# Optimization experiments

Hardware: AMD Instinct MI355X
Metric: run time of the kernel (lower is better)

Reference implementation:

```python
import jax, jax.numpy as jnp
import numpy as np

N_NODES = 50000
N_EDGES = 800000
IN_DIM = 128
HIDDEN = 128
OUT_DIM = 64


def setup_inputs() -> dict:
    key = jax.random.key(0)
    ks = jax.random.split(key, 10)
    x = jax.random.normal(ks[0], (N_NODES, IN_DIM), dtype=jnp.float32)
    edge_index = jax.random.randint(ks[1], (2, N_EDGES), 0, N_NODES, dtype=jnp.int64)
    def lin(k, fan_in, fan_out):
        bound = 1.0 / np.sqrt(fan_in)
        kw, kb = jax.random.split(k)
        W = jax.random.uniform(kw, (fan_in, fan_out), jnp.float32, -bound, bound)
        b = jax.random.uniform(kb, (fan_out,), jnp.float32, -bound, bound)
        return W, b
    W1, b1 = lin(ks[2], IN_DIM, HIDDEN)   # gcn layer 1
    W2, b2 = lin(ks[3], HIDDEN, HIDDEN)   # gcn layer 2
    W3, b3 = lin(ks[4], HIDDEN, HIDDEN)   # post_mp linear 1
    W4, b4 = lin(ks[5], HIDDEN, OUT_DIM)  # post_mp linear 2
    return {"x": x, "edge_index": edge_index,
            "W1": W1, "b1": b1, "W2": W2, "b2": b2,
            "W3": W3, "b3": b3, "W4": W4, "b4": b4}


def reference(x, edge_index, W1, b1, W2, b2, W3, b3, W4, b4):
    N = x.shape[0]
    # add self-loops (matches convert_to_adj)
    loops = jnp.arange(N, dtype=edge_index.dtype)
    row = jnp.concatenate([edge_index[0], loops])  # destination / adj row
    col = jnp.concatenate([edge_index[1], loops])  # source / adj col
    # row-normalization: vals = 1 / deg(row), deg from scatter-add of ones
    deg = jax.ops.segment_sum(jnp.ones(row.shape[0], x.dtype), row, num_segments=N)
    vals = 1.0 / deg[row]  # [E+N]

    def propagate(h):
        # SpMM: out[i] = sum_j A_norm[i,j] * h[j]  via gather-scale-scatter
        return jax.ops.segment_sum(vals[:, None] * h[col], row, num_segments=N)

    # layer 1: spmm -> linear -> relu (dropout is identity in eval mode)
    h = jax.nn.relu(propagate(x) @ W1 + b1)
    # layer 2
    h = jax.nn.relu(propagate(h) @ W2 + b2)
    # post_mp: Linear -> Dropout(eval=identity) -> Linear
    h = h @ W3 + b3
    return h @ W4 + b4
```

## Files before the change

kernel.cpp:

```cpp
#include <hip/hip_runtime.h>
#include <hip/hip_bf16.h>

#define NB 512

typedef __attribute__((ext_vector_type(8))) short short8_t;
typedef __attribute__((ext_vector_type(8))) unsigned short ushort8_t;
typedef __attribute__((ext_vector_type(4))) float f32x4;

__device__ inline unsigned short bf16_rne(float f) {
    union { float f; unsigned u; } x; x.f = f;
    unsigned r = x.u + 0x7fffu + ((x.u >> 16) & 1u);
    return (unsigned short)(r >> 16);
}
__device__ inline float bf16_to_f32(unsigned short h) {
    union { unsigned u; float f; } x; x.u = ((unsigned)h) << 16;
    return x.f;
}


__global__ __launch_bounds__(256) void p0_count_k(const int* __restrict__ e_row, int E, int R,
                                                  int* __restrict__ bucket_cnt) {
    __shared__ int h[NB];
    for (int i = threadIdx.x; i < NB; i += 256) h[i] = 0;
    __syncthreads();
    int base = blockIdx.x * 4096;
#pragma unroll
    for (int j = 0; j < 16; ++j) {
        int i = base + j * 256 + threadIdx.x;
        if (i < E) atomicAdd(&h[e_row[i] / R], 1);
    }
    __syncthreads();
    for (int i = threadIdx.x; i < NB; i += 256)
        if (h[i]) atomicAdd(&bucket_cnt[i], h[i]);
}


__global__ void p0b_scan_k(const int* __restrict__ cnt, int* __restrict__ bptr,
                           int* __restrict__ bcur, int E) {
    __shared__ int s[NB];
    int t = threadIdx.x;
    int v = cnt[t];
    s[t] = v;
    __syncthreads();
    for (int off = 1; off < NB; off <<= 1) {
        int u = (t >= off) ? s[t - off] : 0;
        __syncthreads();
        s[t] += u;
        __syncthreads();
    }
    int excl = s[t] - v;
    bptr[t] = excl;
    bcur[t] = excl;
    if (t == NB - 1) bptr[NB] = E;
}


__global__ __launch_bounds__(256) void p1_scatter_k(const int* __restrict__ er,
                                                    const int* __restrict__ ec, int E, int R,
                                                    int* __restrict__ bcur,
                                                    unsigned* __restrict__ packed) {
    __shared__ int h[NB];
    __shared__ int base[NB];
    for (int i = threadIdx.x; i < NB; i += 256) h[i] = 0;
    __syncthreads();
    int cb = blockIdx.x * 4096;
    int rows[16], cols[16], bks[16];
#pragma unroll
    for (int j = 0; j < 16; ++j) {
        int i = cb + j * 256 + threadIdx.x;
        if (i < E) {
            int r = er[i];
            rows[j] = r;
            cols[j] = ec[i];
            int b = r / R;
            bks[j] = b;
            atomicAdd(&h[b], 1);
        } else {
            bks[j] = -1;
        }
    }
    __syncthreads();
    for (int i = threadIdx.x; i < NB; i += 256)
        base[i] = h[i] ? atomicAdd(&bcur[i], h[i]) : 0;
    __syncthreads();
    for (int i = threadIdx.x; i < NB; i += 256) h[i] = 0;
    __syncthreads();
#pragma unroll
    for (int j = 0; j < 16; ++j) {
        int b = bks[j];
        if (b >= 0) {
            int off = atomicAdd(&h[b], 1);
            packed[base[b] + off] = ((unsigned)(rows[j] - b * R) << 16) | (unsigned)cols[j];
        }
    }
}


__global__ __launch_bounds__(256) void p2_build_k(const unsigned* __restrict__ packed,
                                                  const int* __restrict__ bptr, int R, int N, int E,
                                                  int* __restrict__ row_ptr,
                                                  float* __restrict__ deginv,
                                                  int* __restrict__ csr_col) {
    __shared__ int hist[128];
    __shared__ int excl[129];
    __shared__ int cur[128];
    __shared__ int lcsr[2048];
    int b = blockIdx.x;
    int s = bptr[b], e = bptr[b + 1];
    int m = e - s;
    for (int i = threadIdx.x; i < 128; i += 256) hist[i] = 0;
    __syncthreads();
    for (int i = threadIdx.x; i < m; i += 256) atomicAdd(&hist[packed[s + i] >> 16], 1);
    __syncthreads();
    if (threadIdx.x == 0) {
        int acc = 0;
        for (int r = 0; r < R; ++r) { excl[r] = acc; acc += hist[r]; }
        excl[R] = acc;
    }
    __syncthreads();
    for (int r = threadIdx.x; r < R; r += 256) {
        int gr = b * R + r;
        if (gr < N) {
            row_ptr[gr] = s + excl[r];
            deginv[gr] = 1.0f / (float)(hist[r] + 1);
        }
        cur[r] = excl[r];
    }
    if (b == (int)gridDim.x - 1 && threadIdx.x == 0) row_ptr[N] = E;
    __syncthreads();
    if (m <= 2048) {
        for (int i = threadIdx.x; i < m; i += 256) {
            unsigned pk = packed[s + i];
            int pos = atomicAdd(&cur[pk >> 16], 1);
            lcsr[pos] = (int)(pk & 0xffffu);
        }
        __syncthreads();
        for (int i = threadIdx.x; i < m; i += 256) csr_col[s + i] = lcsr[i];
    } else {
        for (int i = threadIdx.x; i < m; i += 256) {
            unsigned pk = packed[s + i];
            int pos = atomicAdd(&cur[pk >> 16], 1);
            csr_col[s + pos] = (int)(pk & 0xffffu);
        }
    }
}


__global__ void prep_weights_k(const float* __restrict__ W1, const float* __restrict__ W2,
                               const float* __restrict__ W3, const float* __restrict__ b3,
                               const float* __restrict__ W4, const float* __restrict__ b4,
                               unsigned short* __restrict__ w1t, unsigned short* __restrict__ w2t,
                               unsigned short* __restrict__ wft, float* __restrict__ bfv) {
    int idx = blockIdx.x * 256 + threadIdx.x;
    if (idx < 16384) {
        int k = idx >> 7, c = idx & 127;
        w1t[c * 128 + k] = bf16_rne(W1[idx]);
    } else if (idx < 32768) {
        int j = idx - 16384;
        int k = j >> 7, c = j & 127;
        w2t[c * 128 + k] = bf16_rne(W2[j]);
    } else if (idx < 40960) {
        int j = idx - 32768;
        int k = j >> 6, o = j & 63;
        float acc = 0.f;
        for (int m = 0; m < 128; ++m) acc = fmaf(W3[k * 128 + m], W4[m * 64 + o], acc);
        wft[o * 128 + k] = bf16_rne(acc);
    } else if (idx < 41024) {
        int o = idx - 40960;
        float acc = b4[o];
        for (int m = 0; m < 128; ++m) acc = fmaf(b3[m], W4[m * 64 + o], acc);
        bfv[o] = acc;
    }
}


template <int NC, bool OUT_BF16, bool IN_F32>
__global__ __launch_bounds__(256) void gemm_bf16_k(const void* __restrict__ Ain,
                                                   const unsigned short* __restrict__ Wt,
                                                   const float* __restrict__ bias,
                                                   void* __restrict__ Cout, int n) {
    constexpr int CT = NC / 16;
    __shared__ unsigned short As[64 * 128];
    const int t = threadIdx.x;
    const int row0 = blockIdx.x * 64;

    if (IN_F32) {
        const float* A = (const float*)Ain;
#pragma unroll
        for (int it = 0; it < 4; ++it) {
            int idx = it * 2048 + t * 8;
            int rl = idx >> 7;
            int cl = idx & 127;
            int gr = row0 + rl; if (gr > n - 1) gr = n - 1;
            const float4* src = (const float4*)(A + (size_t)gr * 128 + cl);
            float4 v0 = src[0];
            float4 v1 = src[1];
            float f[8] = {v0.x, v0.y, v0.z, v0.w, v1.x, v1.y, v1.z, v1.w};
            ushort8_t vh;
#pragma unroll
            for (int j = 0; j < 8; ++j) vh[j] = bf16_rne(f[j]);
            int byte = rl * 256 + ((cl * 2) ^ ((rl & 7) << 4));
            *(ushort8_t*)((char*)As + byte) = vh;
        }
    } else {
        const char* Ab = (const char*)((const unsigned short*)Ain + (size_t)row0 * 128);
#pragma unroll
        for (int it = 0; it < 4; ++it) {
            int dst = it * 4096 + t * 16;
            int rl = dst >> 8;
            int off = dst & 255;
            int src = rl * 256 + (off ^ ((rl & 7) << 4));
            __builtin_amdgcn_global_load_lds(
                (const __attribute__((address_space(1))) void*)(Ab + src),
                (__attribute__((address_space(3))) void*)((char*)As + dst), 16, 0, 0);
        }
    }
    __syncthreads();

    const int w = t >> 6;
    const int l = t & 63;
    const int col = l & 15;
    const int kg = l >> 4;
    const int arow = w * 16 + col;
    const int abase = arow * 256;
    const int axor = (arow & 7) << 4;

    short8_t afrag[4];
#pragma unroll
    for (int ks = 0; ks < 4; ++ks) {
        int abyte = abase + ((ks * 64 + kg * 16) ^ axor);
        afrag[ks] = *(const short8_t*)((const char*)As + abyte);
    }

    f32x4 acc[CT];
#pragma unroll
    for (int ct = 0; ct < CT; ++ct) acc[ct] = (f32x4){0.f, 0.f, 0.f, 0.f};

#pragma unroll
    for (int ct = 0; ct < CT; ++ct) {
        const unsigned short* wp = Wt + (size_t)(ct * 16 + col) * 128 + kg * 8;
#pragma unroll
        for (int ks = 0; ks < 4; ++ks) {
            short8_t b = *(const short8_t*)(wp + ks * 32);
            acc[ct] = __builtin_amdgcn_mfma_f32_16x16x32_bf16(afrag[ks], b, acc[ct], 0, 0, 0);
        }
    }

    const int orow0 = row0 + w * 16 + kg * 4;
    if (OUT_BF16) {
        unsigned short* C = (unsigned short*)Cout;
#pragma unroll
        for (int ct = 0; ct < CT; ++ct) {
#pragma unroll
            for (int j = 0; j < 4; ++j) {
                C[(size_t)(orow0 + j) * NC + ct * 16 + col] = bf16_rne(acc[ct][j]);
            }
        }
    } else {
        float* C = (float*)Cout;
#pragma unroll
        for (int ct = 0; ct < CT; ++ct) {
            float b = (bias != nullptr) ? bias[ct * 16 + col] : 0.f;
#pragma unroll
            for (int j = 0; j < 4; ++j) {
                int r = orow0 + j;
                if (r < n) C[(size_t)r * NC + ct * 16 + col] = acc[ct][j] + b;
            }
        }
    }
}


__global__ __launch_bounds__(256) void spmm_k(const unsigned short* __restrict__ t,
                                              const int* __restrict__ row_ptr,
                                              const int* __restrict__ csr_col,
                                              const float* __restrict__ deg_inv,
                                              const float* __restrict__ bias,
                                              unsigned short* __restrict__ out, int n) {
    int wave = threadIdx.x >> 6;
    int lane = threadIdx.x & 63;
    int half = lane >> 5;
    int sl = lane & 31;
    int row = blockIdx.x * 8 + wave * 2 + half;
    if (row >= n) return;

    const uint2* tw = (const uint2*)t;
    uint2 sv = tw[(size_t)row * 32 + sl];
    float a0 = bf16_to_f32((unsigned short)(sv.x & 0xffff));
    float a1 = bf16_to_f32((unsigned short)(sv.x >> 16));
    float a2 = bf16_to_f32((unsigned short)(sv.y & 0xffff));
    float a3 = bf16_to_f32((unsigned short)(sv.y >> 16));

    int s = row_ptr[row], e = row_ptr[row + 1];
    int p = s;
    for (; p + 4 <= e; p += 4) {
        int c0 = csr_col[p + 0];
        int c1 = csr_col[p + 1];
        int c2 = csr_col[p + 2];
        int c3 = csr_col[p + 3];
        uint2 v0 = tw[(size_t)c0 * 32 + sl];
        uint2 v1 = tw[(size_t)c1 * 32 + sl];
        uint2 v2 = tw[(size_t)c2 * 32 + sl];
        uint2 v3 = tw[(size_t)c3 * 32 + sl];
        a0 += bf16_to_f32((unsigned short)(v0.x & 0xffff)) + bf16_to_f32((unsigned short)(v1.x & 0xffff)) +
              bf16_to_f32((unsigned short)(v2.x & 0xffff)) + bf16_to_f32((unsigned short)(v3.x & 0xffff));
        a1 += bf16_to_f32((unsigned short)(v0.x >> 16)) + bf16_to_f32((unsigned short)(v1.x >> 16)) +
              bf16_to_f32((unsigned short)(v2.x >> 16)) + bf16_to_f32((unsigned short)(v3.x >> 16));
        a2 += bf16_to_f32((unsigned short)(v0.y & 0xffff)) + bf16_to_f32((unsigned short)(v1.y & 0xffff)) +
              bf16_to_f32((unsigned short)(v2.y & 0xffff)) + bf16_to_f32((unsigned short)(v3.y & 0xffff));
        a3 += bf16_to_f32((unsigned short)(v0.y >> 16)) + bf16_to_f32((unsigned short)(v1.y >> 16)) +
              bf16_to_f32((unsigned short)(v2.y >> 16)) + bf16_to_f32((unsigned short)(v3.y >> 16));
    }
    for (; p < e; ++p) {
        int c = csr_col[p];
        uint2 v = tw[(size_t)c * 32 + sl];
        a0 += bf16_to_f32((unsigned short)(v.x & 0xffff));
        a1 += bf16_to_f32((unsigned short)(v.x >> 16));
        a2 += bf16_to_f32((unsigned short)(v.y & 0xffff));
        a3 += bf16_to_f32((unsigned short)(v.y >> 16));
    }

    float di = deg_inv[row];
    float4 b = ((const float4*)bias)[sl];
    float r0 = fmaxf(fmaf(a0, di, b.x), 0.f);
    float r1 = fmaxf(fmaf(a1, di, b.y), 0.f);
    float r2 = fmaxf(fmaf(a2, di, b.z), 0.f);
    float r3 = fmaxf(fmaf(a3, di, b.w), 0.f);
    uint2 pk;
    pk.x = (unsigned)bf16_rne(r0) | ((unsigned)bf16_rne(r1) << 16);
    pk.y = (unsigned)bf16_rne(r2) | ((unsigned)bf16_rne(r3) << 16);
    ((uint2*)out)[(size_t)row * 32 + sl] = pk;
}


extern "C" void kernel_launch(void* const* d_in, const int* in_sizes, int n_in,
                              void* d_out, int out_size, void* d_ws, size_t ws_size,
                              hipStream_t stream) {
    const float* x  = (const float*)d_in[0];
    const int* edges = (const int*)d_in[1];
    const float* W1 = (const float*)d_in[2];
    const float* b1 = (const float*)d_in[3];
    const float* W2 = (const float*)d_in[4];
    const float* b2 = (const float*)d_in[5];
    const float* W3 = (const float*)d_in[6];
    const float* b3 = (const float*)d_in[7];
    const float* W4 = (const float*)d_in[8];
    const float* b4 = (const float*)d_in[9];

    const int N = in_sizes[0] / 128;
    const int E = in_sizes[1] / 2;
    const int NPAD = (N + 63) & ~63;
    const int R = (N + NB - 1) / NB;
    const int* e_row = edges;
    const int* e_col = edges + E;

    char* p = (char*)d_ws;
    auto alloc = [&](size_t bytes) {
        void* r = (void*)p;
        p += (bytes + 255) & ~(size_t)255;
        return r;
    };
    unsigned short* t_bf = (unsigned short*)alloc((size_t)NPAD * 128 * 2);
    unsigned short* h_bf = (unsigned short*)alloc((size_t)NPAD * 128 * 2);
    float* deginv  = (float*)alloc((size_t)N * 4);
    int*   row_ptr = (int*)alloc((size_t)(N + 1) * 4);
    int*   csr_col = (int*)alloc((size_t)E * 4);
    unsigned* packed = (unsigned*)alloc((size_t)E * 4);
    int*   bucket_cnt = (int*)alloc(NB * 4);
    int*   bucket_ptr = (int*)alloc((NB + 1) * 4);
    int*   bucket_cur = (int*)alloc(NB * 4);
    unsigned short* w1t = (unsigned short*)alloc(128 * 128 * 2);
    unsigned short* w2t = (unsigned short*)alloc(128 * 128 * 2);
    unsigned short* wft = (unsigned short*)alloc(64 * 128 * 2);
    float* bfv     = (float*)alloc(64 * 4);

    float* out = (float*)d_out;

    hipMemsetAsync(bucket_cnt, 0, NB * 4, stream);

    const int echunks = (E + 4095) / 4096;
    p0_count_k<<<echunks, 256, 0, stream>>>(e_row, E, R, bucket_cnt);
    p0b_scan_k<<<1, NB, 0, stream>>>(bucket_cnt, bucket_ptr, bucket_cur, E);
    p1_scatter_k<<<echunks, 256, 0, stream>>>(e_row, e_col, E, R, bucket_cur, packed);
    p2_build_k<<<NB, 256, 0, stream>>>(packed, bucket_ptr, R, N, E, row_ptr, deginv, csr_col);
    prep_weights_k<<<(41024 + 255) / 256, 256, 0, stream>>>(W1, W2, W3, b3, W4, b4,
                                                            w1t, w2t, wft, bfv);

    const int gblocks = NPAD / 64;

    gemm_bf16_k<128, true, true><<<gblocks, 256, 0, stream>>>(x, w1t, nullptr, t_bf, N);
    spmm_k<<<(N + 7) / 8, 256, 0, stream>>>(t_bf, row_ptr, csr_col, deginv, b1, h_bf, N);

    gemm_bf16_k<128, true, false><<<gblocks, 256, 0, stream>>>(h_bf, w2t, nullptr, t_bf, N);
    spmm_k<<<(N + 7) / 8, 256, 0, stream>>>(t_bf, row_ptr, csr_col, deginv, b2, h_bf, N);

    gemm_bf16_k<64, false, false><<<gblocks, 256, 0, stream>>>(h_bf, wft, bfv, out, N);
}
```

Measured before the change: 248.1 us.

## Fuse SpMM aggregation into following GEMM and merge prep kernels

```diff
diff --git a/kernel.cpp b/kernel.cpp
--- a/kernel.cpp
+++ b/kernel.cpp
@@ -18,40 +18,164 @@
 }
 
 
-__global__ __launch_bounds__(256) void p0_count_k(const int* __restrict__ e_row, int E, int R,
-                                                  int* __restrict__ bucket_cnt) {
+template <int NC, bool OUT_BF16>
+__device__ __forceinline__ void gemm_core(const unsigned short* __restrict__ As,
+                                          const unsigned short* __restrict__ Wt,
+                                          const float* __restrict__ gemm_bias,
+                                          void* __restrict__ Cout, int row0, int n) {
+    constexpr int CT = NC / 32;
+    const int t = threadIdx.x;
+    const int w = t >> 6;
+    const int l = t & 63;
+    const int col = l & 15;
+    const int kg = l >> 4;
+    const int arow = (w & 3) * 16 + col;
+    const int cbase = (w >> 2) * (NC / 2);
+    const int abase = arow * 256;
+    const int axor = (arow & 7) << 4;
+
+    short8_t afrag[4];
+#pragma unroll
+    for (int ks = 0; ks < 4; ++ks) {
+        int abyte = abase + ((ks * 64 + kg * 16) ^ axor);
+        afrag[ks] = *(const short8_t*)((const char*)As + abyte);
+    }
+
+    f32x4 acc[CT];
+#pragma unroll
+    for (int ct = 0; ct < CT; ++ct) acc[ct] = (f32x4){0.f, 0.f, 0.f, 0.f};
+
+#pragma unroll
+    for (int ct = 0; ct < CT; ++ct) {
+        const unsigned short* wp = Wt + (size_t)(cbase + ct * 16 + col) * 128 + kg * 8;
+#pragma unroll
+        for (int ks = 0; ks < 4; ++ks) {
+            short8_t b = *(const short8_t*)(wp + ks * 32);
+            acc[ct] = __builtin_amdgcn_mfma_f32_16x16x32_bf16(afrag[ks], b, acc[ct], 0, 0, 0);
+        }
+    }
+
+    const int orow0 = row0 + (w & 3) * 16 + kg * 4;
+    if (OUT_BF16) {
+        unsigned short* C = (unsigned short*)Cout;
+#pragma unroll
+        for (int ct = 0; ct < CT; ++ct) {
+#pragma unroll
+            for (int j = 0; j < 4; ++j) {
+                C[(size_t)(orow0 + j) * NC + cbase + ct * 16 + col] = bf16_rne(acc[ct][j]);
+            }
+        }
+    } else {
+        float* C = (float*)Cout;
+#pragma unroll
+        for (int ct = 0; ct < CT; ++ct) {
+            float b = (gemm_bias != nullptr) ? gemm_bias[cbase + ct * 16 + col] : 0.f;
+#pragma unroll
+            for (int j = 0; j < 4; ++j) {
+                int r = orow0 + j;
+                if (r < n) C[(size_t)r * NC + cbase + ct * 16 + col] = acc[ct][j] + b;
+            }
+        }
+    }
+}
+
+
+__global__ __launch_bounds__(512) void prep_p0_k(const int* __restrict__ e_row, int E, int R,
+                                                 int* __restrict__ bucket_cnt, int pb,
+                                                 const float* __restrict__ W1,
+                                                 const float* __restrict__ W2,
+                                                 const float* __restrict__ W3,
+                                                 const float* __restrict__ b3,
+                                                 const float* __restrict__ W4,
+                                                 const float* __restrict__ b4,
+                                                 unsigned short* __restrict__ w1t,
+                                                 unsigned short* __restrict__ w2t,
+                                                 unsigned short* __restrict__ wft,
+                                                 float* __restrict__ bfv) {
     __shared__ int h[NB];
-    for (int i = threadIdx.x; i < NB; i += 256) h[i] = 0;
-    __syncthreads();
-    int base = blockIdx.x * 4096;
-#pragma unroll
-    for (int j = 0; j < 16; ++j) {
-        int i = base + j * 256 + threadIdx.x;
-        if (i < E) atomicAdd(&h[e_row[i] / R], 1);
-    }
-    __syncthreads();
-    for (int i = threadIdx.x; i < NB; i += 256)
-        if (h[i]) atomicAdd(&bucket_cnt[i], h[i]);
-}
-
-
-__global__ void p0b_scan_k(const int* __restrict__ cnt, int* __restrict__ bptr,
-                           int* __restrict__ bcur, int E) {
-    __shared__ int s[NB];
-    int t = threadIdx.x;
-    int v = cnt[t];
-    s[t] = v;
-    __syncthreads();
-    for (int off = 1; off < NB; off <<= 1) {
-        int u = (t >= off) ? s[t - off] : 0;
+    if ((int)blockIdx.x < pb) {
+        for (int i = threadIdx.x; i < NB; i += 512) h[i] = 0;
         __syncthreads();
-        s[t] += u;
+        int base = blockIdx.x * 8192;
+#pragma unroll
+        for (int j = 0; j < 16; ++j) {
+            int i = base + j * 512 + threadIdx.x;
+            if (i < E) atomicAdd(&h[e_row[i] / R], 1);
+        }
         __syncthreads();
-    }
-    int excl = s[t] - v;
-    bptr[t] = excl;
-    bcur[t] = excl;
-    if (t == NB - 1) bptr[NB] = E;
+        for (int i = threadIdx.x; i < NB; i += 512)
+            if (h[i]) atomicAdd(&bucket_cnt[i], h[i]);
+    } else {
+        int idx = (blockIdx.x - pb) * 512 + threadIdx.x;
+        if (idx < 16384) {
+            int k = idx >> 7, c = idx & 127;
+            w1t[c * 128 + k] = bf16_rne(W1[idx]);
+        } else if (idx < 32768) {
+            int j = idx - 16384;
+            int k = j >> 7, c = j & 127;
+            w2t[c * 128 + k] = bf16_rne(W2[j]);
+        } else if (idx < 40960) {
+            int j = idx - 32768;
+            int k = j >> 6, o = j & 63;
+            float acc = 0.f;
+            for (int m = 0; m < 128; ++m) acc = fmaf(W3[k * 128 + m], W4[m * 64 + o], acc);
+            wft[o * 128 + k] = bf16_rne(acc);
+        } else if (idx < 41024) {
+            int o = idx - 40960;
+            float acc = b4[o];
+            for (int m = 0; m < 128; ++m) acc = fmaf(b3[m], W4[m * 64 + o], acc);
+            bfv[o] = acc;
+        }
+    }
+}
+
+
+__global__ __launch_bounds__(512) void gemm1_p0b_k(const float* __restrict__ x,
+                                                   const unsigned short* __restrict__ w1t,
+                                                   unsigned short* __restrict__ t1, int n, int gb,
+                                                   const int* __restrict__ bucket_cnt,
+                                                   int* __restrict__ bptr, int* __restrict__ bcur,
+                                                   int E) {
+    __shared__ char smem[16384];
+    if ((int)blockIdx.x < gb) {
+        unsigned short* As = (unsigned short*)smem;
+        const int t = threadIdx.x;
+        const int row0 = blockIdx.x * 64;
+#pragma unroll
+        for (int it = 0; it < 2; ++it) {
+            int idx = it * 4096 + t * 8;
+            int rl = idx >> 7;
+            int cl = idx & 127;
+            int gr = row0 + rl; if (gr > n - 1) gr = n - 1;
+            const float4* src = (const float4*)(x + (size_t)gr * 128 + cl);
+            float4 v0 = src[0];
+            float4 v1 = src[1];
+            float f[8] = {v0.x, v0.y, v0.z, v0.w, v1.x, v1.y, v1.z, v1.w};
+            ushort8_t vh;
+#pragma unroll
+            for (int j = 0; j < 8; ++j) vh[j] = bf16_rne(f[j]);
+            int byte = rl * 256 + ((cl * 2) ^ ((rl & 7) << 4));
+            *(ushort8_t*)(smem + byte) = vh;
+        }
+        __syncthreads();
+        gemm_core<128, true>(As, w1t, nullptr, t1, row0, n);
+    } else {
+        int* s = (int*)smem;
+        int t = threadIdx.x;
+        int v = bucket_cnt[t];
+        s[t] = v;
+        __syncthreads();
+        for (int off = 1; off < NB; off <<= 1) {
+            int u = (t >= off) ? s[t - off] : 0;
+            __syncthreads();
+            s[t] += u;
+            __syncthreads();
+        }
+        int excl = s[t] - v;
+        bptr[t] = excl;
+        bcur[t] = excl;
+        if (t == NB - 1) bptr[NB] = E;
+    }
 }
 
 
@@ -146,190 +270,76 @@
 }
 
 
-__global__ void prep_weights_k(const float* __restrict__ W1, const float* __restrict__ W2,
-                               const float* __restrict__ W3, const float* __restrict__ b3,
-                               const float* __restrict__ W4, const float* __restrict__ b4,
-                               unsigned short* __restrict__ w1t, unsigned short* __restrict__ w2t,
-                               unsigned short* __restrict__ wft, float* __restrict__ bfv) {
-    int idx = blockIdx.x * 256 + threadIdx.x;
-    if (idx < 16384) {
-        int k = idx >> 7, c = idx & 127;
-        w1t[c * 128 + k] = bf16_rne(W1[idx]);
-    } else if (idx < 32768) {
-        int j = idx - 16384;
-        int k = j >> 7, c = j & 127;
-        w2t[c * 128 + k] = bf16_rne(W2[j]);
-    } else if (idx < 40960) {
-        int j = idx - 32768;
-        int k = j >> 6, o = j & 63;
-        float acc = 0.f;
-        for (int m = 0; m < 128; ++m) acc = fmaf(W3[k * 128 + m], W4[m * 64 + o], acc);
-        wft[o * 128 + k] = bf16_rne(acc);
-    } else if (idx < 41024) {
-        int o = idx - 40960;
-        float acc = b4[o];
-        for (int m = 0; m < 128; ++m) acc = fmaf(b3[m], W4[m * 64 + o], acc);
-        bfv[o] = acc;
-    }
-}
-
-
-template <int NC, bool OUT_BF16, bool IN_F32>
-__global__ __launch_bounds__(256) void gemm_bf16_k(const void* __restrict__ Ain,
-                                                   const unsigned short* __restrict__ Wt,
-                                                   const float* __restrict__ bias,
-                                                   void* __restrict__ Cout, int n) {
-    constexpr int CT = NC / 16;
+template <int NC, bool OUT_BF16>
+__global__ __launch_bounds__(512) void fused_agg_gemm_k(const unsigned short* __restrict__ tin,
+                                                        const int* __restrict__ row_ptr,
+                                                        const int* __restrict__ csr_col,
+                                                        const float* __restrict__ deginv,
+                                                        const float* __restrict__ agg_bias,
+                                                        const unsigned short* __restrict__ Wt,
+                                                        const float* __restrict__ gemm_bias,
+                                                        void* __restrict__ Cout, int n) {
     __shared__ unsigned short As[64 * 128];
     const int t = threadIdx.x;
     const int row0 = blockIdx.x * 64;
-
-    if (IN_F32) {
-        const float* A = (const float*)Ain;
-#pragma unroll
-        for (int it = 0; it < 4; ++it) {
-            int idx = it * 2048 + t * 8;
-            int rl = idx >> 7;
-            int cl = idx & 127;
-            int gr = row0 + rl; if (gr > n - 1) gr = n - 1;
-            const float4* src = (const float4*)(A + (size_t)gr * 128 + cl);
-            float4 v0 = src[0];
-            float4 v1 = src[1];
-            float f[8] = {v0.x, v0.y, v0.z, v0.w, v1.x, v1.y, v1.z, v1.w};
-            ushort8_t vh;
-#pragma unroll
-            for (int j = 0; j < 8; ++j) vh[j] = bf16_rne(f[j]);
-            int byte = rl * 256 + ((cl * 2) ^ ((rl & 7) << 4));
-            *(ushort8_t*)((char*)As + byte) = vh;
-        }
-    } else {
-        const char* Ab = (const char*)((const unsigned short*)Ain + (size_t)row0 * 128);
-#pragma unroll
-        for (int it = 0; it < 4; ++it) {
-            int dst = it * 4096 + t * 16;
-            int rl = dst >> 8;
-            int off = dst & 255;
-            int src = rl * 256 + (off ^ ((rl & 7) << 4));
-            __builtin_amdgcn_global_load_lds(
-                (const __attribute__((address_space(1))) void*)(Ab + src),
-                (__attribute__((address_space(3))) void*)((char*)As + dst), 16, 0, 0);
-        }
-    }
-    __syncthreads();
-
     const int w = t >> 6;
     const int l = t & 63;
-    const int col = l & 15;
-    const int kg = l >> 4;
-    const int arow = w * 16 + col;
-    const int abase = arow * 256;
-    const int axor = (arow & 7) << 4;
-
-    short8_t afrag[4];
-#pragma unroll
-    for (int ks = 0; ks < 4; ++ks) {
-        int abyte = abase + ((ks * 64 + kg * 16) ^ axor);
-        afrag[ks] = *(const short8_t*)((const char*)As + abyte);
-    }
-
-    f32x4 acc[CT];
-#pragma unroll
-    for (int ct = 0; ct < CT; ++ct) acc[ct] = (f32x4){0.f, 0.f, 0.f, 0.f};
-
-#pragma unroll
-    for (int ct = 0; ct < CT; ++ct) {
-        const unsigned short* wp = Wt + (size_t)(ct * 16 + col) * 128 + kg * 8;
-#pragma unroll
-        for (int ks = 0; ks < 4; ++ks) {
-            short8_t b = *(const short8_t*)(wp + ks * 32);
-            acc[ct] = __builtin_amdgcn_mfma_f32_16x16x32_bf16(afrag[ks], b, acc[ct], 0, 0, 0);
-        }
-    }
-
-    const int orow0 = row0 + w * 16 + kg * 4;
-    if (OUT_BF16) {
-        unsigned short* C = (unsigned short*)Cout;
-#pragma unroll
-        for (int ct = 0; ct < CT; ++ct) {
-#pragma unroll
-            for (int j = 0; j < 4; ++j) {
-                C[(size_t)(orow0 + j) * NC + ct * 16 + col] = bf16_rne(acc[ct][j]);
-            }
-        }
-    } else {
-        float* C = (float*)Cout;
-#pragma unroll
-        for (int ct = 0; ct < CT; ++ct) {
-            float b = (bias != nullptr) ? bias[ct * 16 + col] : 0.f;
-#pragma unroll
-            for (int j = 0; j < 4; ++j) {
-                int r = orow0 + j;
-                if (r < n) C[(size_t)r * NC + ct * 16 + col] = acc[ct][j] + b;
-            }
-        }
-    }
-}
-
-
-__global__ __launch_bounds__(256) void spmm_k(const unsigned short* __restrict__ t,
-                                              const int* __restrict__ row_ptr,
-                                              const int* __restrict__ csr_col,
-                                              const float* __restrict__ deg_inv,
-                                              const float* __restrict__ bias,
-                                              unsigned short* __restrict__ out, int n) {
-    int wave = threadIdx.x >> 6;
-    int lane = threadIdx.x & 63;
-    int half = lane >> 5;
-    int sl = lane & 31;
-    int row = blockIdx.x * 8 + wave * 2 + half;
-    if (row >= n) return;
-
-    const uint2* tw = (const uint2*)t;
-    uint2 sv = tw[(size_t)row * 32 + sl];
-    float a0 = bf16_to_f32((unsigned short)(sv.x & 0xffff));
-    float a1 = bf16_to_f32((unsigned short)(sv.x >> 16));
-    float a2 = bf16_to_f32((unsigned short)(sv.y & 0xffff));
-    float a3 = bf16_to_f32((unsigned short)(sv.y >> 16));
-
-    int s = row_ptr[row], e = row_ptr[row + 1];
-    int p = s;
-    for (; p + 4 <= e; p += 4) {
-        int c0 = csr_col[p + 0];
-        int c1 = csr_col[p + 1];
-        int c2 = csr_col[p + 2];
-        int c3 = csr_col[p + 3];
-        uint2 v0 = tw[(size_t)c0 * 32 + sl];
-        uint2 v1 = tw[(size_t)c1 * 32 + sl];
-        uint2 v2 = tw[(size_t)c2 * 32 + sl];
-        uint2 v3 = tw[(size_t)c3 * 32 + sl];
-        a0 += bf16_to_f32((unsigned short)(v0.x & 0xffff)) + bf16_to_f32((unsigned short)(v1.x & 0xffff)) +
-              bf16_to_f32((unsigned short)(v2.x & 0xffff)) + bf16_to_f32((unsigned short)(v3.x & 0xffff));
-        a1 += bf16_to_f32((unsigned short)(v0.x >> 16)) + bf16_to_f32((unsigned short)(v1.x >> 16)) +
-              bf16_to_f32((unsigned short)(v2.x >> 16)) + bf16_to_f32((unsigned short)(v3.x >> 16));
-        a2 += bf16_to_f32((unsigned short)(v0.y & 0xffff)) + bf16_to_f32((unsigned short)(v1.y & 0xffff)) +
-              bf16_to_f32((unsigned short)(v2.y & 0xffff)) + bf16_to_f32((unsigned short)(v3.y & 0xffff));
-        a3 += bf16_to_f32((unsigned short)(v0.y >> 16)) + bf16_to_f32((unsigned short)(v1.y >> 16)) +
-              bf16_to_f32((unsigned short)(v2.y >> 16)) + bf16_to_f32((unsigned short)(v3.y >> 16));
-    }
-    for (; p < e; ++p) {
-        int c = csr_col[p];
-        uint2 v = tw[(size_t)c * 32 + sl];
-        a0 += bf16_to_f32((unsigned short)(v.x & 0xffff));
-        a1 += bf16_to_f32((unsigned short)(v.x >> 16));
-        a2 += bf16_to_f32((unsigned short)(v.y & 0xffff));
-        a3 += bf16_to_f32((unsigned short)(v.y >> 16));
-    }
-
-    float di = deg_inv[row];
-    float4 b = ((const float4*)bias)[sl];
-    float r0 = fmaxf(fmaf(a0, di, b.x), 0.f);
-    float r1 = fmaxf(fmaf(a1, di, b.y), 0.f);
-    float r2 = fmaxf(fmaf(a2, di, b.z), 0.f);
-    float r3 = fmaxf(fmaf(a3, di, b.w), 0.f);
-    uint2 pk;
-    pk.x = (unsigned)bf16_rne(r0) | ((unsigned)bf16_rne(r1) << 16);
-    pk.y = (unsigned)bf16_rne(r2) | ((unsigned)bf16_rne(r3) << 16);
-    ((uint2*)out)[(size_t)row * 32 + sl] = pk;
+    const int half = l >> 5;
+    const int sl = l & 31;
+    const uint2* tw = (const uint2*)tin;
+    const float4 bb = ((const float4*)agg_bias)[sl];
+
+#pragma unroll
+    for (int it = 0; it < 4; ++it) {
+        int rl = it * 16 + w * 2 + half;
+        int row = row0 + rl; if (row > n - 1) row = n - 1;
+        uint2 sv = tw[(size_t)row * 32 + sl];
+        float a0 = bf16_to_f32((unsigned short)(sv.x & 0xffff));
+        float a1 = bf16_to_f32((unsigned short)(sv.x >> 16));
+        float a2 = bf16_to_f32((unsigned short)(sv.y & 0xffff));
+        float a3 = bf16_to_f32((unsigned short)(sv.y >> 16));
+        int s = row_ptr[row], e = row_ptr[row + 1];
+        int p = s;
+        for (; p + 4 <= e; p += 4) {
+            int c0 = csr_col[p + 0];
+            int c1 = csr_col[p + 1];
+            int c2 = csr_col[p + 2];
+            int c3 = csr_col[p + 3];
+            uint2 v0 = tw[(size_t)c0 * 32 + sl];
+            uint2 v1 = tw[(size_t)c1 * 32 + sl];
+            uint2 v2 = tw[(size_t)c2 * 32 + sl];
+            uint2 v3 = tw[(size_t)c3 * 32 + sl];
+            a0 += bf16_to_f32((unsigned short)(v0.x & 0xffff)) + bf16_to_f32((unsigned short)(v1.x & 0xffff)) +
+                  bf16_to_f32((unsigned short)(v2.x & 0xffff)) + bf16_to_f32((unsigned short)(v3.x & 0xffff));
+            a1 += bf16_to_f32((unsigned short)(v0.x >> 16)) + bf16_to_f32((unsigned short)(v1.x >> 16)) +
+                  bf16_to_f32((unsigned short)(v2.x >> 16)) + bf16_to_f32((unsigned short)(v3.x >> 16));
+            a2 += bf16_to_f32((unsigned short)(v0.y & 0xffff)) + bf16_to_f32((unsigned short)(v1.y & 0xffff)) +
+                  bf16_to_f32((unsigned short)(v2.y & 0xffff)) + bf16_to_f32((unsigned short)(v3.y & 0xffff));
+            a3 += bf16_to_f32((unsigned short)(v0.y >> 16)) + bf16_to_f32((unsigned short)(v1.y >> 16)) +
+                  bf16_to_f32((unsigned short)(v2.y >> 16)) + bf16_to_f32((unsigned short)(v3.y >> 16));
+        }
+        for (; p < e; ++p) {
+            int c = csr_col[p];
+            uint2 v = tw[(size_t)c * 32 + sl];
+            a0 += bf16_to_f32((unsigned short)(v.x & 0xffff));
+            a1 += bf16_to_f32((unsigned short)(v.x >> 16));
+            a2 += bf16_to_f32((unsigned short)(v.y & 0xffff));
+            a3 += bf16_to_f32((unsigned short)(v.y >> 16));
+        }
+        float di = deginv[row];
+        float r0 = fmaxf(fmaf(a0, di, bb.x), 0.f);
+        float r1 = fmaxf(fmaf(a1, di, bb.y), 0.f);
+        float r2 = fmaxf(fmaf(a2, di, bb.z), 0.f);
+        float r3 = fmaxf(fmaf(a3, di, bb.w), 0.f);
+        uint2 pk;
+        pk.x = (unsigned)bf16_rne(r0) | ((unsigned)bf16_rne(r1) << 16);
+        pk.y = (unsigned)bf16_rne(r2) | ((unsigned)bf16_rne(r3) << 16);
+        int byte = rl * 256 + ((sl * 8) ^ ((rl & 7) << 4));
+        *(uint2*)((char*)As + byte) = pk;
+    }
+    __syncthreads();
+
+    gemm_core<NC, OUT_BF16>(As, Wt, gemm_bias, Cout, row0, n);
 }
 
 
@@ -361,7 +371,7 @@
         return r;
     };
     unsigned short* t_bf = (unsigned short*)alloc((size_t)NPAD * 128 * 2);
-    unsigned short* h_bf = (unsigned short*)alloc((size_t)NPAD * 128 * 2);
+    unsigned short* t2_bf = (unsigned short*)alloc((size_t)NPAD * 128 * 2);
     float* deginv  = (float*)alloc((size_t)N * 4);
     int*   row_ptr = (int*)alloc((size_t)(N + 1) * 4);
     int*   csr_col = (int*)alloc((size_t)E * 4);
@@ -378,21 +388,19 @@
 
     hipMemsetAsync(bucket_cnt, 0, NB * 4, stream);
 
-    const int echunks = (E + 4095) / 4096;
-    p0_count_k<<<echunks, 256, 0, stream>>>(e_row, E, R, bucket_cnt);
-    p0b_scan_k<<<1, NB, 0, stream>>>(bucket_cnt, bucket_ptr, bucket_cur, E);
-    p1_scatter_k<<<echunks, 256, 0, stream>>>(e_row, e_col, E, R, bucket_cur, packed);
+    const int PB = (E + 8191) / 8192;
+    const int WB = (41024 + 511) / 512;
+    const int gblocks = NPAD / 64;
+
+    prep_p0_k<<<PB + WB, 512, 0, stream>>>(e_row, E, R, bucket_cnt, PB,
+                                           W1, W2, W3, b3, W4, b4, w1t, w2t, wft, bfv);
+    gemm1_p0b_k<<<gblocks + 1, 512, 0, stream>>>(x, w1t, t_bf, N, gblocks,
+                                                 bucket_cnt, bucket_ptr, bucket_cur, E);
+    p1_scatter_k<<<(E + 4095) / 4096, 256, 0, stream>>>(e_row, e_col, E, R, bucket_cur, packed);
     p2_build_k<<<NB, 256, 0, stream>>>(packed, bucket_ptr, R, N, E, row_ptr, deginv, csr_col);
-    prep_weights_k<<<(41024 + 255) / 256, 256, 0, stream>>>(W1, W2, W3, b3, W4, b4,
-                                                            w1t, w2t, wft, bfv);
-
-    const int gblocks = NPAD / 64;
-
-    gemm_bf16_k<128, true, true><<<gblocks, 256, 0, stream>>>(x, w1t, nullptr, t_bf, N);
-    spmm_k<<<(N + 7) / 8, 256, 0, stream>>>(t_bf, row_ptr, csr_col, deginv, b1, h_bf, N);
-
-    gemm_bf16_k<128, true, false><<<gblocks, 256, 0, stream>>>(h_bf, w2t, nullptr, t_bf, N);
-    spmm_k<<<(N + 7) / 8, 256, 0, stream>>>(t_bf, row_ptr, csr_col, deginv, b2, h_bf, N);
-
-    gemm_bf16_k<64, false, false><<<gblocks, 256, 0, stream>>>(h_bf, wft, bfv, out, N);
-}
+
+    fused_agg_gemm_k<128, true><<<gblocks, 512, 0, stream>>>(
+        t_bf, row_ptr, csr_col, deginv, b1, w2t, nullptr, t2_bf, N);
+    fused_agg_gemm_k<64, false><<<gblocks, 512, 0, stream>>>(
+        t2_bf, row_ptr, csr_col, deginv, b2, wft, bfv, out, N);
+}
```

After: 224.0 us. 1.11x faster.
